# Kernel tuning notes

Measured on AMD Instinct MI355X. Metric: run time of the kernel, lower is better.

## Reference

```python
import jax, jax.numpy as jnp
import numpy as np

N_NODES = 100000
N_EDGES = 1600000
IN_CH = 128
HID = 128
N_GRAPHS = 512


def setup_inputs() -> dict:
    key = jax.random.key(0)
    ks = jax.random.split(key, 16)
    x = jax.random.normal(ks[0], (N_NODES, IN_CH), dtype=jnp.float32)
    edge_index = jax.random.randint(ks[1], (2, N_EDGES), 0, N_NODES, dtype=jnp.int64)
    batch = jnp.sort(jax.random.randint(ks[2], (N_NODES,), 0, N_GRAPHS, dtype=jnp.int64))
    s = 1.0 / np.sqrt(HID)
    params = {
        'W1': jax.random.normal(ks[3], (IN_CH, HID), jnp.float32) / np.sqrt(IN_CH),
        'b1': jnp.zeros((HID,), jnp.float32),
        'W2': jax.random.normal(ks[4], (HID, HID), jnp.float32) * s,
        'b2': jnp.zeros((HID,), jnp.float32),
        'W3': jax.random.normal(ks[5], (HID, HID), jnp.float32) * s,
        'b3': jnp.zeros((HID,), jnp.float32),
        'Wf1': jax.random.normal(ks[6], (2 * HID, HID), jnp.float32) / np.sqrt(2 * HID),
        'bf1': jnp.zeros((HID,), jnp.float32),
        'Wf2': jax.random.normal(ks[7], (HID, HID // 2), jnp.float32) * s,
        'bf2': jnp.zeros((HID // 2,), jnp.float32),
        'Wf3': jax.random.normal(ks[8], (HID // 2, 1), jnp.float32) / np.sqrt(HID // 2),
        'bf3': jnp.zeros((1,), jnp.float32),
    }
    return {'x': x, 'edge_index': edge_index, 'batch': batch, 'n_graphs': N_GRAPHS, **params}


def _gcn_norm(edge_index, n_nodes):
    # add self-loops, then symmetric normalization D^{-1/2} (A+I) D^{-1/2}
    loops = jnp.arange(n_nodes, dtype=edge_index.dtype)
    src = jnp.concatenate([edge_index[0], loops])
    dst = jnp.concatenate([edge_index[1], loops])
    deg = jax.ops.segment_sum(jnp.ones_like(dst, dtype=jnp.float32), dst, num_segments=n_nodes)
    dinv = jnp.where(deg > 0, jax.lax.rsqrt(deg), 0.0)
    norm = dinv[src] * dinv[dst]  # [E + N]
    return src, dst, norm


def _gcn_conv(h, W, b, src, dst, norm, n_nodes):
    h = h @ W                                   # [N, H]
    msg = h[src] * norm[:, None]                # gather + edge scale
    agg = jax.ops.segment_sum(msg, dst, num_segments=n_nodes)  # scatter-add
    return agg + b


def reference(x, edge_index, batch, n_graphs, W1, b1, W2, b2, W3, b3, Wf1, bf1, Wf2, bf2, Wf3, bf3):
    n_nodes = x.shape[0]
    src, dst, norm = _gcn_norm(edge_index, n_nodes)

    h = jax.nn.relu(_gcn_conv(x, W1, b1, src, dst, norm, n_nodes))
    h_res = h
    h = jax.nn.relu(_gcn_conv(h, W2, b2, src, dst, norm, n_nodes)) + h_res
    h_res = h
    h = jax.nn.relu(_gcn_conv(h, W3, b3, src, dst, norm, n_nodes)) + h_res

    ones = jnp.ones((n_nodes, 1), jnp.float32)
    counts = jax.ops.segment_sum(ones, batch, num_segments=n_graphs)  # [G,1]
    g_mean = jax.ops.segment_sum(h, batch, num_segments=n_graphs) / jnp.maximum(counts, 1.0)
    g_max = jax.ops.segment_max(h, batch, num_segments=n_graphs)
    g = jnp.concatenate([g_mean, g_max], axis=1)  # [G, 2H]

    # MLP head (dropout is identity at inference)
    g = jax.nn.relu(g @ Wf1 + bf1)
    g = jax.nn.relu(g @ Wf2 + bf2)
    return g @ Wf3 + bf3  # [G, 1]
```

## Files before the change

kernel.cpp:

```cpp
#include <hip/hip_runtime.h>
#include <hip/hip_bf16.h>

#define NBMAX 256
#define BSH 9
#define BMSK 511
#define CHUNK 4096
#define NCAP 10240

typedef __attribute__((ext_vector_type(8))) short short8;
typedef __attribute__((ext_vector_type(4))) float f32x4;

__device__ inline unsigned short bf16_rne(float x) {
    unsigned u = __float_as_uint(x);
    u = (u + 0x7FFFu + ((u >> 16) & 1u)) >> 16;
    return (unsigned short)u;
}
__device__ inline float bf16_to_f(unsigned short h) {
    return __uint_as_float(((unsigned)h) << 16);
}
__device__ inline void split2(float v, short& h, short& lo) {
    unsigned short hb = bf16_rne(v);
    h = (short)hb;
    lo = (short)bf16_rne(v - bf16_to_f(hb));
}


__global__ __launch_bounds__(256) void k_bcnt(const int* __restrict__ dst, int E, int NB,
                                              int* __restrict__ bucket_cnt) {
    __shared__ int lcnt[NBMAX];
    int t = threadIdx.x;
    int base = blockIdx.x * CHUNK;
    for (int i = t; i < NB; i += 256) lcnt[i] = 0;
    __syncthreads();
#pragma unroll
    for (int i = 0; i < 16; i++) {
        int e = base + i * 256 + t;
        if (e < E) atomicAdd(&lcnt[dst[e] >> BSH], 1);
    }
    __syncthreads();
    for (int i = t; i < NB; i += 256) {
        int c = lcnt[i];
        if (c) atomicAdd(&bucket_cnt[i], c);
    }
}

__global__ __launch_bounds__(256) void k_bscan(const int* __restrict__ bucket_cnt,
                                               int NB, int E, int N,
                                               int* __restrict__ bucket_off,
                                               int* __restrict__ bcur,
                                               int* __restrict__ rowstart) {
    __shared__ int sh[NBMAX];
    int t = threadIdx.x;
    int v = (t < NB) ? bucket_cnt[t] : 0;
    sh[t] = v;
    __syncthreads();
    for (int off = 1; off < NBMAX; off <<= 1) {
        int x = (t >= off) ? sh[t - off] : 0;
        __syncthreads();
        sh[t] += x;
        __syncthreads();
    }
    if (t < NB) {
        int excl = sh[t] - v;
        bucket_off[t] = excl;
        bcur[t] = excl;
    }
    if (t == 0) {
        bucket_off[NB] = E;
        rowstart[N] = E;
    }
}

__global__ __launch_bounds__(256) void k_bucket(const int* __restrict__ src,
                                                const int* __restrict__ dst, int E, int NB,
                                                int* __restrict__ bcur,
                                                unsigned* __restrict__ pairs) {
    __shared__ int lcnt[NBMAX];
    __shared__ int loff[NBMAX];
    __shared__ int gbase[NBMAX];
    __shared__ unsigned plds[CHUNK];
    __shared__ unsigned char blds[CHUNK];
    int t = threadIdx.x;
    int base = blockIdx.x * CHUNK;
    for (int i = t; i < NBMAX; i += 256) lcnt[i] = 0;
    __syncthreads();
    int rank[16], bid[16];
    unsigned pk[16];
#pragma unroll
    for (int i = 0; i < 16; i++) {
        int e = base + i * 256 + t;
        if (e < E) {
            int d = dst[e];
            int b = d >> BSH;
            bid[i] = b;
            pk[i] = ((unsigned)(d & BMSK) << 17) | (unsigned)src[e];
            rank[i] = atomicAdd(&lcnt[b], 1);
        } else bid[i] = -1;
    }
    __syncthreads();
    loff[t] = lcnt[t];
    __syncthreads();
    for (int off = 1; off < NBMAX; off <<= 1) {
        int x = (t >= off) ? loff[t - off] : 0;
        __syncthreads();
        loff[t] += x;
        __syncthreads();
    }
    if (t < NB) {
        int c = lcnt[t];
        gbase[t] = c ? atomicAdd(&bcur[t], c) : 0;
    }
    __syncthreads();
#pragma unroll
    for (int i = 0; i < 16; i++) {
        int b = bid[i];
        if (b >= 0) {
            int pos = loff[b] - lcnt[b] + rank[i];
            plds[pos] = pk[i];
            blds[pos] = (unsigned char)b;
        }
    }
    __syncthreads();
    int total = min(E - base, CHUNK);
    for (int i = t; i < total; i += 256) {
        int b = blds[i];
        int local = i - (loff[b] - lcnt[b]);
        pairs[gbase[b] + local] = plds[i];
    }
}

__global__ __launch_bounds__(512) void k_node(const unsigned* __restrict__ pairs,
                                              const int* __restrict__ bucket_off, int N,
                                              int* __restrict__ rowstart,
                                              float* __restrict__ dinv,
                                              int* __restrict__ csr_src) {
    __shared__ int cnt_l[512];
    __shared__ int cur_l[512];
    __shared__ int wsum[8];
    __shared__ int stage[NCAP];
    int t = threadIdx.x;
    int lane = t & 63, wv = t >> 6;
    int b = blockIdx.x;
    int n0 = b << BSH;
    int nn = min(512, N - n0);
    cnt_l[t] = 0;
    __syncthreads();
    int e0 = bucket_off[b], e1 = bucket_off[b + 1];
    int len = e1 - e0;
    for (int e = e0 + t; e < e1; e += 512) {
        atomicAdd(&cnt_l[pairs[e] >> 17], 1);
    }
    __syncthreads();
    int c = cnt_l[t];
    int v = c;
#pragma unroll
    for (int off = 1; off < 64; off <<= 1) {
        int x = __shfl_up(v, off);
        if (lane >= off) v += x;
    }
    if (lane == 63) wsum[wv] = v;
    __syncthreads();
    if (t < 8) {
        int wval = wsum[t];
#pragma unroll
        for (int off = 1; off < 8; off <<= 1) {
            int x = __shfl_up(wval, off);
            if (lane >= off) wval += x;
        }
        wsum[t] = wval;
    }
    __syncthreads();
    int prefix = (wv > 0) ? wsum[wv - 1] : 0;
    int start = e0 + prefix + v - c;
    if (t < nn) {
        rowstart[n0 + t] = start;
        dinv[n0 + t] = rsqrtf((float)c + 1.0f);
    }
    if (len <= NCAP) {
        cur_l[t] = start - e0;
        __syncthreads();
        for (int e = e0 + t; e < e1; e += 512) {
            unsigned p = pairs[e];
            int r = atomicAdd(&cur_l[p >> 17], 1);
            stage[r] = (int)(p & 0x1FFFFu);
        }
        __syncthreads();
        for (int i = t; i < len; i += 512) csr_src[e0 + i] = stage[i];
    } else {
        cur_l[t] = start;
        __syncthreads();
        for (int e = e0 + t; e < e1; e += 512) {
            unsigned p = pairs[e];
            int r = atomicAdd(&cur_l[p >> 17], 1);
            csr_src[r] = (int)(p & 0x1FFFFu);
        }
    }
}

__global__ __launch_bounds__(256) void k_wprep3(const float* __restrict__ W1,
                                                const float* __restrict__ W2,
                                                const float* __restrict__ W3,
                                                unsigned short* __restrict__ WH,
                                                unsigned short* __restrict__ WL,
                                                int* __restrict__ bucket_cnt) {
    if (blockIdx.x == 0 && threadIdx.x < NBMAX) bucket_cnt[threadIdx.x] = 0;
    int wi = blockIdx.x >> 6;
    int idx = (blockIdx.x & 63) * 256 + threadIdx.x;
    const float* W = (wi == 0) ? W1 : (wi == 1) ? W2 : W3;
    int j = idx & 7;
    int lane = (idx >> 3) & 63;
    int ct = (idx >> 9) & 7;
    int kc = idx >> 12;
    int k = kc * 32 + (lane >> 4) * 8 + j;
    int col = ct * 16 + (lane & 15);
    float v = W[k * 128 + col];
    unsigned short hb = bf16_rne(v);
    WH[wi * 16384 + idx] = hb;
    WL[wi * 16384 + idx] = bf16_rne(v - bf16_to_f(hb));
}


__global__ __launch_bounds__(256) void k_gemm3(const float* __restrict__ A,
                                               const unsigned short* __restrict__ WH,
                                               const unsigned short* __restrict__ WL,
                                               const float* __restrict__ dinv,
                                               unsigned short* __restrict__ U, int N) {
    int wv = threadIdx.x >> 6;
    int l = threadIdx.x & 63;
    int quad = l >> 4;
    int lm = l & 15;
    int rowBase = blockIdx.x * 128 + wv * 32;

    f32x4 acc[2][8] = {};

    int r0 = rowBase + lm;
    int r1 = rowBase + 16 + lm;

    for (int kc = 0; kc < 4; kc++) {
        int k0 = kc * 32 + quad * 8;
        float av0[8] = {}, av1[8] = {};
        if (r0 < N) {
            float4 a = *(const float4*)&A[(size_t)r0 * 128 + k0];
            float4 b = *(const float4*)&A[(size_t)r0 * 128 + k0 + 4];
            av0[0] = a.x; av0[1] = a.y; av0[2] = a.z; av0[3] = a.w;
            av0[4] = b.x; av0[5] = b.y; av0[6] = b.z; av0[7] = b.w;
        }
        if (r1 < N) {
            float4 a = *(const float4*)&A[(size_t)r1 * 128 + k0];
            float4 b = *(const float4*)&A[(size_t)r1 * 128 + k0 + 4];
            av1[0] = a.x; av1[1] = a.y; av1[2] = a.z; av1[3] = a.w;
            av1[4] = b.x; av1[5] = b.y; av1[6] = b.z; av1[7] = b.w;
        }
        short8 ah0, al0, ah1, al1;
#pragma unroll
        for (int j = 0; j < 8; j++) {
            short h, lo;
            split2(av0[j], h, lo); ah0[j] = h; al0[j] = lo;
            split2(av1[j], h, lo); ah1[j] = h; al1[j] = lo;
        }
#pragma unroll
        for (int ct = 0; ct < 8; ct++) {
            size_t fo = ((size_t)(kc * 8 + ct) * 64 + l) * 8;
            short8 wh = *(const short8*)&WH[fo];
            short8 wl = *(const short8*)&WL[fo];
            acc[0][ct] = __builtin_amdgcn_mfma_f32_16x16x32_bf16(ah0, wh, acc[0][ct], 0, 0, 0);
            acc[0][ct] = __builtin_amdgcn_mfma_f32_16x16x32_bf16(ah0, wl, acc[0][ct], 0, 0, 0);
            acc[0][ct] = __builtin_amdgcn_mfma_f32_16x16x32_bf16(al0, wh, acc[0][ct], 0, 0, 0);
            acc[1][ct] = __builtin_amdgcn_mfma_f32_16x16x32_bf16(ah1, wh, acc[1][ct], 0, 0, 0);
            acc[1][ct] = __builtin_amdgcn_mfma_f32_16x16x32_bf16(ah1, wl, acc[1][ct], 0, 0, 0);
            acc[1][ct] = __builtin_amdgcn_mfma_f32_16x16x32_bf16(al1, wh, acc[1][ct], 0, 0, 0);
        }
    }

#pragma unroll
    for (int rt = 0; rt < 2; rt++) {
#pragma unroll
        for (int reg = 0; reg < 4; reg++) {
            int row = rowBase + rt * 16 + quad * 4 + reg;
            if (row < N) {
                float dv = dinv[row];
#pragma unroll
                for (int ct = 0; ct < 8; ct++) {
                    U[(size_t)row * 128 + ct * 16 + lm] = bf16_rne(dv * acc[rt][ct][reg]);
                }
            }
        }
    }
}


template <int RES>
__global__ __launch_bounds__(256) void k_agg(const unsigned short* __restrict__ U,
                                             const int* __restrict__ rowstart,
                                             const int* __restrict__ csr_src,
                                             const float* __restrict__ dinv,
                                             const float* __restrict__ bias,
                                             float* __restrict__ H, int N) {
    int wave = threadIdx.x >> 6;
    int lane = threadIdx.x & 63;
    int n = blockIdx.x * 4 + wave;
    if (n >= N) return;
    int grp = lane >> 4;
    int li = lane & 15;
    int e0 = rowstart[n], e1 = rowstart[n + 1];
    int len = e1 - e0;
    int q0 = e0 + ((len * grp) >> 2);
    int q1 = e0 + ((len * (grp + 1)) >> 2);

    float a0 = 0.f, a1 = 0.f, a2 = 0.f, a3 = 0.f;
    float a4 = 0.f, a5 = 0.f, a6 = 0.f, a7 = 0.f;
    float b0 = 0.f, b1 = 0.f, b2 = 0.f, b3 = 0.f;
    float b4 = 0.f, b5 = 0.f, b6 = 0.f, b7 = 0.f;

    int e = q0;
    for (; e + 2 <= q1; e += 2) {
        int s0 = csr_src[e];
        int s1 = csr_src[e + 1];
        uint4 r0 = *(const uint4*)&U[(size_t)s0 * 128 + li * 8];
        uint4 r1 = *(const uint4*)&U[(size_t)s1 * 128 + li * 8];
        a0 += __uint_as_float(r0.x << 16);        a1 += __uint_as_float(r0.x & 0xFFFF0000u);
        a2 += __uint_as_float(r0.y << 16);        a3 += __uint_as_float(r0.y & 0xFFFF0000u);
        a4 += __uint_as_float(r0.z << 16);        a5 += __uint_as_float(r0.z & 0xFFFF0000u);
        a6 += __uint_as_float(r0.w << 16);        a7 += __uint_as_float(r0.w & 0xFFFF0000u);
        b0 += __uint_as_float(r1.x << 16);        b1 += __uint_as_float(r1.x & 0xFFFF0000u);
        b2 += __uint_as_float(r1.y << 16);        b3 += __uint_as_float(r1.y & 0xFFFF0000u);
        b4 += __uint_as_float(r1.z << 16);        b5 += __uint_as_float(r1.z & 0xFFFF0000u);
        b6 += __uint_as_float(r1.w << 16);        b7 += __uint_as_float(r1.w & 0xFFFF0000u);
    }
    if (e < q1) {
        int s0 = csr_src[e];
        uint4 r0 = *(const uint4*)&U[(size_t)s0 * 128 + li * 8];
        a0 += __uint_as_float(r0.x << 16);        a1 += __uint_as_float(r0.x & 0xFFFF0000u);
        a2 += __uint_as_float(r0.y << 16);        a3 += __uint_as_float(r0.y & 0xFFFF0000u);
        a4 += __uint_as_float(r0.z << 16);        a5 += __uint_as_float(r0.z & 0xFFFF0000u);
        a6 += __uint_as_float(r0.w << 16);        a7 += __uint_as_float(r0.w & 0xFFFF0000u);
    }
    a0 += b0; a1 += b1; a2 += b2; a3 += b3;
    a4 += b4; a5 += b5; a6 += b6; a7 += b7;

    a0 += __shfl_xor(a0, 16); a1 += __shfl_xor(a1, 16);
    a2 += __shfl_xor(a2, 16); a3 += __shfl_xor(a3, 16);
    a4 += __shfl_xor(a4, 16); a5 += __shfl_xor(a5, 16);
    a6 += __shfl_xor(a6, 16); a7 += __shfl_xor(a7, 16);
    a0 += __shfl_xor(a0, 32); a1 += __shfl_xor(a1, 32);
    a2 += __shfl_xor(a2, 32); a3 += __shfl_xor(a3, 32);
    a4 += __shfl_xor(a4, 32); a5 += __shfl_xor(a5, 32);
    a6 += __shfl_xor(a6, 32); a7 += __shfl_xor(a7, 32);

    if (grp == 0) {
        uint4 qs = *(const uint4*)&U[(size_t)n * 128 + li * 8];
        float4 bi0 = *(const float4*)&bias[li * 8];
        float4 bi1 = *(const float4*)&bias[li * 8 + 4];
        float dn = dinv[n];
        float4 o0, o1v;
        o0.x = fmaxf(dn * (a0 + __uint_as_float(qs.x << 16)) + bi0.x, 0.f);
        o0.y = fmaxf(dn * (a1 + __uint_as_float(qs.x & 0xFFFF0000u)) + bi0.y, 0.f);
        o0.z = fmaxf(dn * (a2 + __uint_as_float(qs.y << 16)) + bi0.z, 0.f);
        o0.w = fmaxf(dn * (a3 + __uint_as_float(qs.y & 0xFFFF0000u)) + bi0.w, 0.f);
        o1v.x = fmaxf(dn * (a4 + __uint_as_float(qs.z << 16)) + bi1.x, 0.f);
        o1v.y = fmaxf(dn * (a5 + __uint_as_float(qs.z & 0xFFFF0000u)) + bi1.y, 0.f);
        o1v.z = fmaxf(dn * (a6 + __uint_as_float(qs.w << 16)) + bi1.z, 0.f);
        o1v.w = fmaxf(dn * (a7 + __uint_as_float(qs.w & 0xFFFF0000u)) + bi1.w, 0.f);
        size_t hi = (size_t)n * 128 + li * 8;
        if (RES) {
            float4 h0 = *(const float4*)&H[hi];
            float4 h1 = *(const float4*)&H[hi + 4];
            o0.x += h0.x; o0.y += h0.y; o0.z += h0.z; o0.w += h0.w;
            o1v.x += h1.x; o1v.y += h1.y; o1v.z += h1.z; o1v.w += h1.w;
        }
        *(float4*)&H[hi] = o0;
        *(float4*)&H[hi + 4] = o1v;
    }
}


__global__ __launch_bounds__(256) void k_head(const float* __restrict__ H,
                                              const int* __restrict__ batch, int N, int G,
                                              const float* __restrict__ Wf1,
                                              const float* __restrict__ bf1,
                                              const float* __restrict__ Wf2,
                                              const float* __restrict__ bf2,
                                              const float* __restrict__ Wf3,
                                              const float* __restrict__ bf3,
                                              float* __restrict__ out) {
    __shared__ float ssum[256];
    __shared__ float smax[256];
    __shared__ float grow[256];
    __shared__ float o1[128];
    __shared__ float o2[64];
    int g = blockIdx.x;
    int t = threadIdx.x;
    int i0, i1;
    {
        int lo = 0, hi = N;
        while (lo < hi) { int m = (lo + hi) >> 1; if (batch[m] < g) lo = m + 1; else hi = m; }
        i0 = lo;
        lo = i0; hi = N;
        while (lo < hi) { int m = (lo + hi) >> 1; if (batch[m] < g + 1) lo = m + 1; else hi = m; }
        i1 = lo;
    }
    int c = t & 127;
    int half = t >> 7;
    int cn = i1 - i0;
    int mid = i0 + (cn >> 1);
    int a0 = half ? mid : i0;
    int a1 = half ? i1 : mid;
    float s = 0.f, m = -3.4e38f;
    for (int i = a0; i < a1; i++) {
        float v = H[(size_t)i * 128 + c];
        s += v;
        m = fmaxf(m, v);
    }
    ssum[t] = s;
    smax[t] = m;
    __syncthreads();
    if (half == 0) {
        float st = ssum[c] + ssum[c + 128];
        float mt = fmaxf(smax[c], smax[c + 128]);
        grow[c] = (cn > 0) ? st / (float)cn : 0.f;
        grow[128 + c] = (cn > 0) ? mt : 0.f;
    }
    __syncthreads();
    if (t < 128) {
        float acc = bf1[t];
#pragma unroll 8
        for (int k = 0; k < 256; k++) acc = fmaf(grow[k], Wf1[k * 128 + t], acc);
        o1[t] = fmaxf(acc, 0.f);
    }
    __syncthreads();
    if (t < 64) {
        float a2 = bf2[t];
#pragma unroll 8
        for (int k = 0; k < 128; k++) a2 = fmaf(o1[k], Wf2[k * 64 + t], a2);
        o2[t] = fmaxf(a2, 0.f);
    }
    __syncthreads();
    if (t < 64) {
        float p = o2[t] * Wf3[t];
        for (int off = 32; off > 0; off >>= 1) p += __shfl_down(p, off);
        if (t == 0) out[g] = p + bf3[0];
    }
}


extern "C" void kernel_launch(void* const* d_in, const int* in_sizes, int n_in,
                              void* d_out, int out_size, void* d_ws, size_t ws_size,
                              hipStream_t stream) {
    const float* x = (const float*)d_in[0];
    const int* ei = (const int*)d_in[1];
    const int* batch = (const int*)d_in[2];
    const float* W1 = (const float*)d_in[4];
    const float* b1 = (const float*)d_in[5];
    const float* W2 = (const float*)d_in[6];
    const float* b2 = (const float*)d_in[7];
    const float* W3 = (const float*)d_in[8];
    const float* b3 = (const float*)d_in[9];
    const float* Wf1 = (const float*)d_in[10];
    const float* bf1 = (const float*)d_in[11];
    const float* Wf2 = (const float*)d_in[12];
    const float* bf2 = (const float*)d_in[13];
    const float* Wf3 = (const float*)d_in[14];
    const float* bf3 = (const float*)d_in[15];

    const int N = in_sizes[0] / 128;
    const int E = in_sizes[1] / 2;
    const int G = out_size;

    const int* src = ei;
    const int* dst = ei + E;

    char* w = (char*)d_ws;
    size_t off = 0;
    auto alloc = [&](size_t bytes) -> void* {
        void* p = w + off;
        off += (bytes + 255) / 256 * 256;
        return p;
    };
    unsigned short* U = (unsigned short*)alloc((size_t)N * 128 * 2);
    float* H = (float*)alloc((size_t)N * 128 * 4);
    unsigned* pairs = (unsigned*)alloc((size_t)E * 4);
    int* csr_src = (int*)alloc((size_t)E * 4);
    int* rowstart = (int*)alloc((size_t)(N + 1) * 4);
    float* dinv = (float*)alloc((size_t)N * 4);
    int* bucket_cnt = (int*)alloc(NBMAX * 4);
    int* bucket_off = (int*)alloc((NBMAX + 1) * 4);
    int* bcur = (int*)alloc(NBMAX * 4);
    unsigned short* WH = (unsigned short*)alloc(3 * 16384 * 2);
    unsigned short* WL = (unsigned short*)alloc(3 * 16384 * 2);
    float* out = (float*)d_out;

    const int NB = (N + BMSK) >> BSH;
    const int ebk = (E + CHUNK - 1) / CHUNK;

    k_wprep3<<<dim3(192), dim3(256), 0, stream>>>(W1, W2, W3, WH, WL, bucket_cnt);

    k_bcnt<<<dim3(ebk), dim3(256), 0, stream>>>(dst, E, NB, bucket_cnt);
    k_bscan<<<dim3(1), dim3(NBMAX), 0, stream>>>(bucket_cnt, NB, E, N, bucket_off, bcur, rowstart);
    k_bucket<<<dim3(ebk), dim3(256), 0, stream>>>(src, dst, E, NB, bcur, pairs);
    k_node<<<dim3(NB), dim3(512), 0, stream>>>(pairs, bucket_off, N, rowstart, dinv, csr_src);

    const int gemmGrid = (N + 127) / 128;
    const int aggGrid = (N + 3) / 4;

    k_gemm3<<<dim3(gemmGrid), dim3(256), 0, stream>>>(x, WH, WL, dinv, U, N);
    k_agg<0><<<dim3(aggGrid), dim3(256), 0, stream>>>(U, rowstart, csr_src, dinv, b1, H, N);
    k_gemm3<<<dim3(gemmGrid), dim3(256), 0, stream>>>(H, WH + 16384, WL + 16384, dinv, U, N);
    k_agg<1><<<dim3(aggGrid), dim3(256), 0, stream>>>(U, rowstart, csr_src, dinv, b2, H, N);
    k_gemm3<<<dim3(gemmGrid), dim3(256), 0, stream>>>(H, WH + 32768, WL + 32768, dinv, U, N);
    k_agg<1><<<dim3(aggGrid), dim3(256), 0, stream>>>(U, rowstart, csr_src, dinv, b3, H, N);

    k_head<<<dim3(G), dim3(256), 0, stream>>>(H, batch, N, G, Wf1, bf1, Wf2, bf2, Wf3, bf3, out);
}
```

Before: 500.0 us.

## Store hidden activations as pre-split bf16 hi/lo pairs for GEMM input

The aggregation kernel now writes each hidden feature as two bf16 halves (hi and lo) instead of fp32. The following GEMM loads these halves directly rather than splitting fp32 on the fly, and the residual add and pooling head reconstruct the values from hi+lo. Memory traffic is unchanged because hi+lo is the same size as fp32, so the saving is the split arithmetic in the GEMM. The head also moves to 512 threads, splitting each graph's node range four ways instead of two. The hi+lo pair carries slightly less precision than fp32.

```diff
diff --git a/kernel.cpp b/kernel.cpp
--- a/kernel.cpp
+++ b/kernel.cpp
@@ -220,11 +220,14 @@
 }
 
 
-__global__ __launch_bounds__(256) void k_gemm3(const float* __restrict__ A,
-                                               const unsigned short* __restrict__ WH,
-                                               const unsigned short* __restrict__ WL,
-                                               const float* __restrict__ dinv,
-                                               unsigned short* __restrict__ U, int N) {
+template <int SPLITIN>
+__device__ __forceinline__ void gemm3_core(const float* __restrict__ A,
+                                           const unsigned short* __restrict__ AH,
+                                           const unsigned short* __restrict__ AL,
+                                           const unsigned short* __restrict__ WH,
+                                           const unsigned short* __restrict__ WL,
+                                           const float* __restrict__ dinv,
+                                           unsigned short* __restrict__ U, int N) {
     int wv = threadIdx.x >> 6;
     int l = threadIdx.x & 63;
     int quad = l >> 4;
@@ -238,25 +241,36 @@
 
     for (int kc = 0; kc < 4; kc++) {
         int k0 = kc * 32 + quad * 8;
-        float av0[8] = {}, av1[8] = {};
-        if (r0 < N) {
-            float4 a = *(const float4*)&A[(size_t)r0 * 128 + k0];
-            float4 b = *(const float4*)&A[(size_t)r0 * 128 + k0 + 4];
-            av0[0] = a.x; av0[1] = a.y; av0[2] = a.z; av0[3] = a.w;
-            av0[4] = b.x; av0[5] = b.y; av0[6] = b.z; av0[7] = b.w;
-        }
-        if (r1 < N) {
-            float4 a = *(const float4*)&A[(size_t)r1 * 128 + k0];
-            float4 b = *(const float4*)&A[(size_t)r1 * 128 + k0 + 4];
-            av1[0] = a.x; av1[1] = a.y; av1[2] = a.z; av1[3] = a.w;
-            av1[4] = b.x; av1[5] = b.y; av1[6] = b.z; av1[7] = b.w;
-        }
-        short8 ah0, al0, ah1, al1;
-#pragma unroll
-        for (int j = 0; j < 8; j++) {
-            short h, lo;
-            split2(av0[j], h, lo); ah0[j] = h; al0[j] = lo;
-            split2(av1[j], h, lo); ah1[j] = h; al1[j] = lo;
+        short8 ah0 = {}, al0 = {}, ah1 = {}, al1 = {};
+        if (SPLITIN) {
+            if (r0 < N) {
+                ah0 = *(const short8*)&AH[(size_t)r0 * 128 + k0];
+                al0 = *(const short8*)&AL[(size_t)r0 * 128 + k0];
+            }
+            if (r1 < N) {
+                ah1 = *(const short8*)&AH[(size_t)r1 * 128 + k0];
+                al1 = *(const short8*)&AL[(size_t)r1 * 128 + k0];
+            }
+        } else {
+            float av0[8] = {}, av1[8] = {};
+            if (r0 < N) {
+                float4 a = *(const float4*)&A[(size_t)r0 * 128 + k0];
+                float4 b = *(const float4*)&A[(size_t)r0 * 128 + k0 + 4];
+                av0[0] = a.x; av0[1] = a.y; av0[2] = a.z; av0[3] = a.w;
+                av0[4] = b.x; av0[5] = b.y; av0[6] = b.z; av0[7] = b.w;
+            }
+            if (r1 < N) {
+                float4 a = *(const float4*)&A[(size_t)r1 * 128 + k0];
+                float4 b = *(const float4*)&A[(size_t)r1 * 128 + k0 + 4];
+                av1[0] = a.x; av1[1] = a.y; av1[2] = a.z; av1[3] = a.w;
+                av1[4] = b.x; av1[5] = b.y; av1[6] = b.z; av1[7] = b.w;
+            }
+#pragma unroll
+            for (int j = 0; j < 8; j++) {
+                short h, lo;
+                split2(av0[j], h, lo); ah0[j] = h; al0[j] = lo;
+                split2(av1[j], h, lo); ah1[j] = h; al1[j] = lo;
+            }
         }
 #pragma unroll
         for (int ct = 0; ct < 8; ct++) {
@@ -288,6 +302,23 @@
     }
 }
 
+__global__ __launch_bounds__(256) void k_gemm3f(const float* __restrict__ A,
+                                                const unsigned short* __restrict__ WH,
+                                                const unsigned short* __restrict__ WL,
+                                                const float* __restrict__ dinv,
+                                                unsigned short* __restrict__ U, int N) {
+    gemm3_core<0>(A, nullptr, nullptr, WH, WL, dinv, U, N);
+}
+
+__global__ __launch_bounds__(256) void k_gemm3s(const unsigned short* __restrict__ AH,
+                                                const unsigned short* __restrict__ AL,
+                                                const unsigned short* __restrict__ WH,
+                                                const unsigned short* __restrict__ WL,
+                                                const float* __restrict__ dinv,
+                                                unsigned short* __restrict__ U, int N) {
+    gemm3_core<1>(nullptr, AH, AL, WH, WL, dinv, U, N);
+}
+
 
 template <int RES>
 __global__ __launch_bounds__(256) void k_agg(const unsigned short* __restrict__ U,
@@ -295,7 +326,8 @@
                                              const int* __restrict__ csr_src,
                                              const float* __restrict__ dinv,
                                              const float* __restrict__ bias,
-                                             float* __restrict__ H, int N) {
+                                             unsigned short* __restrict__ HH,
+                                             unsigned short* __restrict__ HL, int N) {
     int wave = threadIdx.x >> 6;
     int lane = threadIdx.x & 63;
     int n = blockIdx.x * 4 + wave;
@@ -352,29 +384,46 @@
         float4 bi0 = *(const float4*)&bias[li * 8];
         float4 bi1 = *(const float4*)&bias[li * 8 + 4];
         float dn = dinv[n];
-        float4 o0, o1v;
-        o0.x = fmaxf(dn * (a0 + __uint_as_float(qs.x << 16)) + bi0.x, 0.f);
-        o0.y = fmaxf(dn * (a1 + __uint_as_float(qs.x & 0xFFFF0000u)) + bi0.y, 0.f);
-        o0.z = fmaxf(dn * (a2 + __uint_as_float(qs.y << 16)) + bi0.z, 0.f);
-        o0.w = fmaxf(dn * (a3 + __uint_as_float(qs.y & 0xFFFF0000u)) + bi0.w, 0.f);
-        o1v.x = fmaxf(dn * (a4 + __uint_as_float(qs.z << 16)) + bi1.x, 0.f);
-        o1v.y = fmaxf(dn * (a5 + __uint_as_float(qs.z & 0xFFFF0000u)) + bi1.y, 0.f);
-        o1v.z = fmaxf(dn * (a6 + __uint_as_float(qs.w << 16)) + bi1.z, 0.f);
-        o1v.w = fmaxf(dn * (a7 + __uint_as_float(qs.w & 0xFFFF0000u)) + bi1.w, 0.f);
+        float v0 = fmaxf(dn * (a0 + __uint_as_float(qs.x << 16)) + bi0.x, 0.f);
+        float v1 = fmaxf(dn * (a1 + __uint_as_float(qs.x & 0xFFFF0000u)) + bi0.y, 0.f);
+        float v2 = fmaxf(dn * (a2 + __uint_as_float(qs.y << 16)) + bi0.z, 0.f);
+        float v3 = fmaxf(dn * (a3 + __uint_as_float(qs.y & 0xFFFF0000u)) + bi0.w, 0.f);
+        float v4 = fmaxf(dn * (a4 + __uint_as_float(qs.z << 16)) + bi1.x, 0.f);
+        float v5 = fmaxf(dn * (a5 + __uint_as_float(qs.z & 0xFFFF0000u)) + bi1.y, 0.f);
+        float v6 = fmaxf(dn * (a6 + __uint_as_float(qs.w << 16)) + bi1.z, 0.f);
+        float v7 = fmaxf(dn * (a7 + __uint_as_float(qs.w & 0xFFFF0000u)) + bi1.w, 0.f);
         size_t hi = (size_t)n * 128 + li * 8;
         if (RES) {
-            float4 h0 = *(const float4*)&H[hi];
-            float4 h1 = *(const float4*)&H[hi + 4];
-            o0.x += h0.x; o0.y += h0.y; o0.z += h0.z; o0.w += h0.w;
-            o1v.x += h1.x; o1v.y += h1.y; o1v.z += h1.z; o1v.w += h1.w;
-        }
-        *(float4*)&H[hi] = o0;
-        *(float4*)&H[hi + 4] = o1v;
-    }
-}
-
-
-__global__ __launch_bounds__(256) void k_head(const float* __restrict__ H,
+            uint4 rh = *(const uint4*)&HH[hi];
+            uint4 rl = *(const uint4*)&HL[hi];
+            v0 += __uint_as_float(rh.x << 16) + __uint_as_float(rl.x << 16);
+            v1 += __uint_as_float(rh.x & 0xFFFF0000u) + __uint_as_float(rl.x & 0xFFFF0000u);
+            v2 += __uint_as_float(rh.y << 16) + __uint_as_float(rl.y << 16);
+            v3 += __uint_as_float(rh.y & 0xFFFF0000u) + __uint_as_float(rl.y & 0xFFFF0000u);
+            v4 += __uint_as_float(rh.z << 16) + __uint_as_float(rl.z << 16);
+            v5 += __uint_as_float(rh.z & 0xFFFF0000u) + __uint_as_float(rl.z & 0xFFFF0000u);
+            v6 += __uint_as_float(rh.w << 16) + __uint_as_float(rl.w << 16);
+            v7 += __uint_as_float(rh.w & 0xFFFF0000u) + __uint_as_float(rl.w & 0xFFFF0000u);
+        }
+        float vv[8] = {v0, v1, v2, v3, v4, v5, v6, v7};
+        unsigned hw[4], lw[4];
+#pragma unroll
+        for (int j = 0; j < 4; j++) {
+            unsigned short h0 = bf16_rne(vv[2 * j]);
+            unsigned short h1 = bf16_rne(vv[2 * j + 1]);
+            unsigned short l0 = bf16_rne(vv[2 * j] - bf16_to_f(h0));
+            unsigned short l1 = bf16_rne(vv[2 * j + 1] - bf16_to_f(h1));
+            hw[j] = (unsigned)h0 | ((unsigned)h1 << 16);
+            lw[j] = (unsigned)l0 | ((unsigned)l1 << 16);
+        }
+        *(uint4*)&HH[hi] = make_uint4(hw[0], hw[1], hw[2], hw[3]);
+        *(uint4*)&HL[hi] = make_uint4(lw[0], lw[1], lw[2], lw[3]);
+    }
+}
+
+
+__global__ __launch_bounds__(512) void k_head(const unsigned short* __restrict__ HH,
+                                              const unsigned short* __restrict__ HL,
                                               const int* __restrict__ batch, int N, int G,
                                               const float* __restrict__ Wf1,
                                               const float* __restrict__ bf1,
@@ -383,8 +432,8 @@
                                               const float* __restrict__ Wf3,
                                               const float* __restrict__ bf3,
                                               float* __restrict__ out) {
-    __shared__ float ssum[256];
-    __shared__ float smax[256];
+    __shared__ float ssum[512];
+    __shared__ float smax[512];
     __shared__ float grow[256];
     __shared__ float o1[128];
     __shared__ float o2[64];
@@ -400,23 +449,23 @@
         i1 = lo;
     }
     int c = t & 127;
-    int half = t >> 7;
+    int sl = t >> 7;
     int cn = i1 - i0;
-    int mid = i0 + (cn >> 1);
-    int a0 = half ? mid : i0;
-    int a1 = half ? i1 : mid;
+    int a0 = i0 + ((cn * sl) >> 2);
+    int a1 = i0 + ((cn * (sl + 1)) >> 2);
     float s = 0.f, m = -3.4e38f;
     for (int i = a0; i < a1; i++) {
-        float v = H[(size_t)i * 128 + c];
+        size_t idx = (size_t)i * 128 + c;
+        float v = bf16_to_f(HH[idx]) + bf16_to_f(HL[idx]);
         s += v;
         m = fmaxf(m, v);
     }
     ssum[t] = s;
     smax[t] = m;
     __syncthreads();
-    if (half == 0) {
-        float st = ssum[c] + ssum[c + 128];
-        float mt = fmaxf(smax[c], smax[c + 128]);
+    if (t < 128) {
+        float st = ssum[c] + ssum[c + 128] + ssum[c + 256] + ssum[c + 384];
+        float mt = fmaxf(fmaxf(smax[c], smax[c + 128]), fmaxf(smax[c + 256], smax[c + 384]));
         grow[c] = (cn > 0) ? st / (float)cn : 0.f;
         grow[128 + c] = (cn > 0) ? mt : 0.f;
     }
@@ -477,7 +526,8 @@
         return p;
     };
     unsigned short* U = (unsigned short*)alloc((size_t)N * 128 * 2);
-    float* H = (float*)alloc((size_t)N * 128 * 4);
+    unsigned short* HHp = (unsigned short*)alloc((size_t)N * 128 * 2);
+    unsigned short* HLp = (unsigned short*)alloc((size_t)N * 128 * 2);
     unsigned* pairs = (unsigned*)alloc((size_t)E * 4);
     int* csr_src = (int*)alloc((size_t)E * 4);
     int* rowstart = (int*)alloc((size_t)(N + 1) * 4);
@@ -502,12 +552,12 @@
     const int gemmGrid = (N + 127) / 128;
     const int aggGrid = (N + 3) / 4;
 
-    k_gemm3<<<dim3(gemmGrid), dim3(256), 0, stream>>>(x, WH, WL, dinv, U, N);
-    k_agg<0><<<dim3(aggGrid), dim3(256), 0, stream>>>(U, rowstart, csr_src, dinv, b1, H, N);
-    k_gemm3<<<dim3(gemmGrid), dim3(256), 0, stream>>>(H, WH + 16384, WL + 16384, dinv, U, N);
-    k_agg<1><<<dim3(aggGrid), dim3(256), 0, stream>>>(U, rowstart, csr_src, dinv, b2, H, N);
-    k_gemm3<<<dim3(gemmGrid), dim3(256), 0, stream>>>(H, WH + 32768, WL + 32768, dinv, U, N);
-    k_agg<1><<<dim3(aggGrid), dim3(256), 0, stream>>>(U, rowstart, csr_src, dinv, b3, H, N);
-
-    k_head<<<dim3(G), dim3(256), 0, stream>>>(H, batch, N, G, Wf1, bf1, Wf2, bf2, Wf3, bf3, out);
-}
+    k_gemm3f<<<dim3(gemmGrid), dim3(256), 0, stream>>>(x, WH, WL, dinv, U, N);
+    k_agg<0><<<dim3(aggGrid), dim3(256), 0, stream>>>(U, rowstart, csr_src, dinv, b1, HHp, HLp, N);
+    k_gemm3s<<<dim3(gemmGrid), dim3(256), 0, stream>>>(HHp, HLp, WH + 16384, WL + 16384, dinv, U, N);
+    k_agg<1><<<dim3(aggGrid), dim3(256), 0, stream>>>(U, rowstart, csr_src, dinv, b2, HHp, HLp, N);
+    k_gemm3s<<<dim3(gemmGrid), dim3(256), 0, stream>>>(HHp, HLp, WH + 32768, WL + 32768, dinv, U, N);
+    k_agg<1><<<dim3(aggGrid), dim3(256), 0, stream>>>(U, rowstart, csr_src, dinv, b3, HHp, HLp, N);
+
+    k_head<<<dim3(G), dim3(512), 0, stream>>>(HHp, HLp, batch, N, G, Wf1, bf1, Wf2, bf2, Wf3, bf3, out);
+}
```

After: 494.8 us. Within noise of the previous version (-1.0%).
